# Optimization experiments

Measured on AMD Instinct MI355X. Metric: run time of the kernel, lower is better.

## Reference

```python
import jax, jax.numpy as jnp
import numpy as np

B, S, H = 32, 64, 512
ATT = 128


def _window_index_tables(seq_len):
    # Enumerate all contiguous windows of size 2..S, same set (order-independent
    # for the softmax-weighted sum) as the torch double loop.
    starts, ends = [], []
    for w in range(2, seq_len + 1):
        for s in range(0, seq_len - w + 1):
            starts.append(s)
            ends.append(s + w)
    starts = np.asarray(starts, np.int32)
    ends = np.asarray(ends, np.int32)
    widths = ends - starts
    ks = np.floor(np.log2(widths)).astype(np.int32)  # sparse-table level per window
    e2 = ends - (1 << ks)                            # second gather position
    return starts, e2, ks


def setup_inputs() -> dict:
    key = jax.random.key(0)
    k0, k1, k2, k3, k4 = jax.random.split(key, 5)
    return {
        "lstm_out": jax.random.normal(k0, (B, S, H), dtype=jnp.float32),
        "W1": jax.random.normal(k1, (H, ATT), dtype=jnp.float32) * 0.05,
        "b1": jax.random.normal(k2, (ATT,), dtype=jnp.float32) * 0.05,
        "W2": jax.random.normal(k3, (ATT, 1), dtype=jnp.float32) * 0.05,
        "b2": jax.random.normal(k4, (1,), dtype=jnp.float32) * 0.05,
    }


def reference(lstm_out, W1, b1, W2, b2):
    b, s, h = lstm_out.shape
    # Sparse table: M[k][:, i] = max over lstm_out[:, i : i+2^k] (clipped to s).
    n_levels = int(np.floor(np.log2(s))) + 1
    tables = [lstm_out]
    for k in range(1, n_levels):
        half = 1 << (k - 1)
        prev = tables[-1]
        shifted = jnp.concatenate(
            [prev[:, half:], jnp.full((b, half, h), -jnp.inf, prev.dtype)], axis=1)
        tables.append(jnp.maximum(prev, shifted))
    Mstack = jnp.stack(tables)  # [K, B, S, H]

    starts, e2, ks = _window_index_tables(s)
    # Range max of each window = max of two overlapping power-of-two blocks.
    pooled = jnp.maximum(Mstack[ks, :, starts], Mstack[ks, :, e2])  # [n_win, B, H]
    pooled = jnp.transpose(pooled, (1, 0, 2))  # [B, n_win, H]

    hid = jax.nn.relu(jnp.einsum("bnh,ha->bna", pooled, W1) + b1)
    scores = jnp.einsum("bna,ao->bno", hid, W2) + b2  # [B, n_win, 1]
    attn = jax.nn.softmax(scores, axis=1)
    return jnp.sum(attn * pooled, axis=1)  # [B, H]
```

## Files before the change

kernel.cpp:

```cpp
#include <hip/hip_runtime.h>
#include <stdint.h>


typedef unsigned short u16;
typedef unsigned int u32;

#define B_    32
#define S_    64
#define H_    512
#define ATT_  128
#define NWIN  2016
#define NLEV  7
#define TLEV  6

typedef __bf16 bf16x8 __attribute__((ext_vector_type(8)));
typedef float  f32x4  __attribute__((ext_vector_type(4)));

__device__ __forceinline__ float asf(u32 i) {
  union { u32 i; float f; } v; v.i = i; return v.f;
}
__device__ __forceinline__ u32 asu(float f) {
  union { float f; u32 i; } v; v.f = f; return v.i;
}
__device__ __forceinline__ float bf2f(u16 u) { return asf(((u32)u) << 16); }
__device__ __forceinline__ u16 f2bf(float f) {
  u32 i = asu(f);
  i += 0x7fffu + ((i >> 16) & 1u);
  return (u16)(i >> 16);
}
__device__ __forceinline__ u32 bfmax2(u32 a, u32 b) {
  float a0 = asf(a << 16), a1 = asf(a & 0xffff0000u);
  float b0 = asf(b << 16), b1 = asf(b & 0xffff0000u);
  u32 m0 = asu(fmaxf(a0, b0)), m1 = asu(fmaxf(a1, b1));
  return (m1 & 0xffff0000u) | (m0 >> 16);
}
__device__ __forceinline__ uint4 bfmax8(uint4 a, uint4 b) {
  uint4 m;
  m.x = bfmax2(a.x, b.x); m.y = bfmax2(a.y, b.y);
  m.z = bfmax2(a.z, b.z); m.w = bfmax2(a.w, b.w);
  return m;
}
__device__ __forceinline__ bf16x8 as_bf16x8(uint4 v) {
  union { uint4 u; bf16x8 h; } c; c.u = v; return c.h;
}

__launch_bounds__(256)
__global__ void k01_init(const float* __restrict__ lstm, const float* __restrict__ W1,
                         u16* __restrict__ table, u16* __restrict__ w1tf,
                         u16* __restrict__ widx) {
  int bid = blockIdx.x, tid = threadIdx.x;
  __shared__ u16 bufA[64 * 64], bufB[64 * 64];
  if (bid < 256) {
    int hc = bid & 7, b = bid >> 3;
    const float* src = lstm + (size_t)b * S_ * H_ + hc * 64;
    u16* tb = table + (size_t)b * TLEV * S_ * H_ + hc * 64;
    for (int t = tid; t < 64 * 16; t += 256) {
      int r = t >> 4, c4 = t & 15;
      float4 f = *reinterpret_cast<const float4*>(src + r * H_ + c4 * 4);
      ushort4 u;
      u.x = f2bf(f.x); u.y = f2bf(f.y); u.z = f2bf(f.z); u.w = f2bf(f.w);
      *reinterpret_cast<ushort4*>(&bufA[r * 64 + c4 * 4]) = u;
    }
    u16* pa = bufA; u16* pb = bufB;
    for (int k = 1; k < NLEV; ++k) {
      __syncthreads();
      int half = 1 << (k - 1);
      u16* dst_g = tb + (size_t)(k - 1) * S_ * H_;
      for (int t = tid; t < 64 * 16; t += 256) {
        int r = t >> 4, c4 = t & 15;
        int r2 = r + half; if (r2 > 63) r2 = 63;
        uint2 a  = *reinterpret_cast<const uint2*>(&pa[r  * 64 + c4 * 4]);
        uint2 bq = *reinterpret_cast<const uint2*>(&pa[r2 * 64 + c4 * 4]);
        uint2 m; m.x = bfmax2(a.x, bq.x); m.y = bfmax2(a.y, bq.y);
        *reinterpret_cast<uint2*>(&pb[r * 64 + c4 * 4]) = m;
        *reinterpret_cast<uint2*>(dst_g + r * H_ + c4 * 4) = m;
      }
      u16* tmp = pa; pa = pb; pb = tmp;
    }
  } else {
    int gb = bid - 256;
    if (gb == 0) {
      for (int n = tid; n < NWIN; n += 256) {
        int w = 2, rem = n;
        while (rem >= 65 - w) { rem -= 65 - w; ++w; }
        int s = rem;
        int k = 31 - __clz(w);
        int e2 = s + w - (1 << k);
        widx[n] = (u16)(s | (e2 << 6) | (k << 12));
      }
    }
    for (int q = tid; q < 2048; q += 256) {
      int idx = gb * 2048 + q;
      int e = idx & 7, L = (idx >> 3) & 63, j = (idx >> 9) & 7;
      int k2i = (idx >> 12) & 1, kc = idx >> 13;
      int n  = j * 16 + (L & 15);
      int kq = kc * 64 + k2i * 32 + (L >> 4) * 8 + e;
      w1tf[idx] = f2bf(W1[kq * ATT_ + n]);
    }
  }
}

__launch_bounds__(256)
__attribute__((amdgpu_waves_per_eu(1, 4)))
__global__ void k2_scores(const u16* __restrict__ table, const u16* __restrict__ w1tf,
                          const float* __restrict__ b1, const float* __restrict__ w2,
                          const u16* __restrict__ widx, float* __restrict__ scores) {
  const int b = blockIdx.y, mt = blockIdx.x;
  __shared__ u16 Ts[128 * 64];
  __shared__ u16 Bs[8192];
  __shared__ u16 widx_l[64];
  __shared__ float b1s[128], w2s[128];
  int tid = threadIdx.x;
  if (tid < 64) {
    int n = mt * 64 + tid; if (n > NWIN - 1) n = NWIN - 1;
    widx_l[tid] = widx[n];
  }
  if (tid < 128) { b1s[tid] = b1[tid]; w2s[tid] = w2[tid]; }
  __syncthreads();

  const int lv_lo = widx_l[0] >> 12;
  const u16* tb = table + (size_t)b * TLEV * S_ * H_ + (size_t)(lv_lo - 1) * S_ * H_;

  int t0 = tid, t1 = tid + 256, t2 = tid + 512, t3 = tid + 768;
  int r0 = t0 >> 3, r1 = t1 >> 3, r2 = t2 >> 3, r3 = t3 >> 3;
  int c0 = t0 & 7,  c1 = t1 & 7,  c2 = t2 & 7,  c3 = t3 & 7;
  const u16* ts0 = tb + r0 * H_ + c0 * 8;
  const u16* ts1 = tb + r1 * H_ + c1 * 8;
  const u16* ts2 = tb + r2 * H_ + c2 * 8;
  const u16* ts3 = tb + r3 * H_ + c3 * 8;
  int sd0 = r0 * 64 + ((c0 ^ (r0 & 7)) * 8);
  int sd1 = r1 * 64 + ((c1 ^ (r1 & 7)) * 8);
  int sd2 = r2 * 64 + ((c2 ^ (r2 & 7)) * 8);
  int sd3 = r3 * 64 + ((c3 ^ (r3 & 7)) * 8);
  int bo0 = tid * 8, bo1 = bo0 + 2048, bo2 = bo0 + 4096, bo3 = bo0 + 6144;

  int wid = tid >> 6, lane = tid & 63;
  int lrow = lane & 15, quad = lane >> 4;

  int aoff[2][2];
  {
    int pk = widx_l[wid * 16 + lrow];
    int s = pk & 63, e2 = (pk >> 6) & 63, lv = (pk >> 12) - lv_lo;
    int rs = lv * 64 + s, re = lv * 64 + e2;
#pragma unroll
    for (int k2i = 0; k2i < 2; ++k2i) {
      int c = quad + k2i * 4;
      aoff[k2i][0] = rs * 64 + ((c ^ (rs & 7)) * 8);
      aoff[k2i][1] = re * 64 + ((c ^ (re & 7)) * 8);
    }
  }

  uint4 rT0, rT1, rT2, rT3, rB0, rB1, rB2, rB3;

#define ISSUE(KC) do { \
  int kk_ = (KC) * 64; \
  const u16* wsrc_ = w1tf + (KC) * 8192; \
  rT0 = *reinterpret_cast<const uint4*>(ts0 + kk_); \
  rT1 = *reinterpret_cast<const uint4*>(ts1 + kk_); \
  rT2 = *reinterpret_cast<const uint4*>(ts2 + kk_); \
  rT3 = *reinterpret_cast<const uint4*>(ts3 + kk_); \
  rB0 = *reinterpret_cast<const uint4*>(wsrc_ + bo0); \
  rB1 = *reinterpret_cast<const uint4*>(wsrc_ + bo1); \
  rB2 = *reinterpret_cast<const uint4*>(wsrc_ + bo2); \
  rB3 = *reinterpret_cast<const uint4*>(wsrc_ + bo3); \
} while (0)

#define STAGE() do { \
  *reinterpret_cast<uint4*>(&Ts[sd0]) = rT0; \
  *reinterpret_cast<uint4*>(&Ts[sd1]) = rT1; \
  *reinterpret_cast<uint4*>(&Ts[sd2]) = rT2; \
  *reinterpret_cast<uint4*>(&Ts[sd3]) = rT3; \
  *reinterpret_cast<uint4*>(&Bs[bo0]) = rB0; \
  *reinterpret_cast<uint4*>(&Bs[bo1]) = rB1; \
  *reinterpret_cast<uint4*>(&Bs[bo2]) = rB2; \
  *reinterpret_cast<uint4*>(&Bs[bo3]) = rB3; \
} while (0)

  ISSUE(0);

  f32x4 acc[8];
#pragma unroll
  for (int j = 0; j < 8; ++j) acc[j] = (f32x4){0.f, 0.f, 0.f, 0.f};

  for (int kc = 0; kc < 8; ++kc) {
    __syncthreads();
    STAGE();
    __syncthreads();
    if (kc < 7) ISSUE(kc + 1);
#pragma unroll
    for (int k2i = 0; k2i < 2; ++k2i) {
      uint4 va = *reinterpret_cast<const uint4*>(&Ts[aoff[k2i][0]]);
      uint4 vb = *reinterpret_cast<const uint4*>(&Ts[aoff[k2i][1]]);
      bf16x8 af = as_bf16x8(bfmax8(va, vb));
      const u16* bk = &Bs[k2i * 4096 + lane * 8];
#pragma unroll
      for (int j = 0; j < 8; ++j) {
        bf16x8 bfr = *reinterpret_cast<const bf16x8*>(bk + j * 512);
        acc[j] = __builtin_amdgcn_mfma_f32_16x16x32_bf16(af, bfr, acc[j], 0, 0, 0);
      }
    }
  }

#undef ISSUE
#undef STAGE

#pragma unroll
  for (int r = 0; r < 4; ++r) {
    float p = 0.f;
#pragma unroll
    for (int j = 0; j < 8; ++j) {
      int n = j * 16 + lrow;
      float v = acc[j][r] + b1s[n];
      p += (v > 0.f ? v : 0.f) * w2s[n];
    }
    p += __shfl_xor(p, 1, 16);
    p += __shfl_xor(p, 2, 16);
    p += __shfl_xor(p, 4, 16);
    p += __shfl_xor(p, 8, 16);
    if (lrow == 0) {
      int nw = mt * 64 + wid * 16 + quad * 4 + r;
      if (nw < NWIN) scores[b * NWIN + nw] = p;
    }
  }
}

__launch_bounds__(256)
__global__ void k34_out(const u16* __restrict__ table, const float* __restrict__ scores,
                        const u16* __restrict__ widx, float* __restrict__ out) {
  int hc = blockIdx.x, b = blockIdx.y, tid = threadIdx.x;
  __shared__ u16 Tl[6 * 64 * 16];
  __shared__ float attn_l[NWIN];
  __shared__ u16 widx_l[NWIN];
  __shared__ float red[16][16];
  __shared__ float wredM[4], wredS[4];
  const u16* tb = table + (size_t)b * TLEV * S_ * H_;
  int h0 = hc * 16;
  int lane = tid & 63, wid = tid >> 6;

  for (int t = tid; t < 6 * 64 * 2; t += 256) {
    int row = t >> 1, c = t & 1;
    uint4 v = *reinterpret_cast<const uint4*>(tb + row * H_ + h0 + c * 8);
    *reinterpret_cast<uint4*>(&Tl[row * 16 + c * 8]) = v;
  }
  for (int n = tid; n < NWIN; n += 256) widx_l[n] = widx[n];

  float mx = -1e30f;
  for (int n = tid; n < NWIN; n += 256) {
    float v = scores[b * NWIN + n];
    attn_l[n] = v;
    mx = fmaxf(mx, v);
  }
#pragma unroll
  for (int off = 32; off > 0; off >>= 1) mx = fmaxf(mx, __shfl_xor(mx, off, 64));
  if (lane == 0) wredM[wid] = mx;
  __syncthreads();
  mx = fmaxf(fmaxf(wredM[0], wredM[1]), fmaxf(wredM[2], wredM[3]));
  float sum = 0.f;
  for (int n = tid; n < NWIN; n += 256) {
    float e = __expf(attn_l[n] - mx);
    attn_l[n] = e;
    sum += e;
  }
#pragma unroll
  for (int off = 32; off > 0; off >>= 1) sum += __shfl_xor(sum, off, 64);
  if (lane == 0) wredS[wid] = sum;
  __syncthreads();
  float inv = 1.f / (wredS[0] + wredS[1] + wredS[2] + wredS[3]);

  int h = tid & 15, g = tid >> 4;
  float acc = 0.f;
  for (int n = g * 126; n < g * 126 + 126; ++n) {
    int pk = widx_l[n];
    int s = pk & 63, e2 = (pk >> 6) & 63, lv = pk >> 12;
    float va = bf2f(Tl[((lv - 1) * 64 + s) * 16 + h]);
    float vb = bf2f(Tl[((lv - 1) * 64 + e2) * 16 + h]);
    acc += attn_l[n] * fmaxf(va, vb);
  }
  red[g][h] = acc;
  __syncthreads();
  if (tid < 16) {
    float s2 = 0.f;
#pragma unroll
    for (int g2 = 0; g2 < 16; ++g2) s2 += red[g2][tid];
    out[b * H_ + h0 + tid] = s2 * inv;
  }
}

extern "C" void kernel_launch(void* const* d_in, const int* in_sizes, int n_in,
                              void* d_out, int out_size, void* d_ws, size_t ws_size,
                              hipStream_t stream) {
  const float* lstm = (const float*)d_in[0];
  const float* W1   = (const float*)d_in[1];
  const float* b1   = (const float*)d_in[2];
  const float* W2   = (const float*)d_in[3];
  float* out = (float*)d_out;

  char* ws = (char*)d_ws;
  u16*   widx   = (u16*)(ws + 0);
  u16*   w1tf   = (u16*)(ws + 4096);
  u16*   table  = (u16*)(ws + 135168);
  float* scores = (float*)(ws + 12718080);

  k01_init <<<288, 256, 0, stream>>>(lstm, W1, table, w1tf, widx);
  k2_scores<<<dim3(32, B_), 256, 0, stream>>>(table, w1tf, b1, W2, widx, scores);
  k34_out  <<<dim3(32, B_), 256, 0, stream>>>(table, scores, widx, out);
}
```

Measured before the change: 118.1 us.

## Retile score GEMM to 128 windows per block with 2x4 wave grid

The scoring kernel now processes 128 windows per block with 512 threads, arranged as a 4x2 grid of waves (M by N halves). Each wave computes two 16-row M fragments against four N fragments. The per-wave partial scores are combined through shared memory before the store. This halves the number of times each W1 chunk is reloaded per batch and reuses each B fragment across two A fragments. In exchange it has half as many blocks, larger blocks and a higher register count per thread, plus an extra barrier and reduction at the end.

```diff
diff --git a/kernel.cpp b/kernel.cpp
--- a/kernel.cpp
+++ b/kernel.cpp
@@ -100,7 +100,7 @@
   }
 }
 
-__launch_bounds__(256)
+__launch_bounds__(512)
 __attribute__((amdgpu_waves_per_eu(1, 4)))
 __global__ void k2_scores(const u16* __restrict__ table, const u16* __restrict__ w1tf,
                           const float* __restrict__ b1, const float* __restrict__ w2,
@@ -108,79 +108,72 @@
   const int b = blockIdx.y, mt = blockIdx.x;
   __shared__ u16 Ts[128 * 64];
   __shared__ u16 Bs[8192];
-  __shared__ u16 widx_l[64];
+  __shared__ u16 widx_l[128];
   __shared__ float b1s[128], w2s[128];
+  __shared__ float sc2[2][128];
   int tid = threadIdx.x;
-  if (tid < 64) {
-    int n = mt * 64 + tid; if (n > NWIN - 1) n = NWIN - 1;
+  if (tid < 128) {
+    int n = mt * 128 + tid; if (n > NWIN - 1) n = NWIN - 1;
     widx_l[tid] = widx[n];
-  }
-  if (tid < 128) { b1s[tid] = b1[tid]; w2s[tid] = w2[tid]; }
+    b1s[tid] = b1[tid]; w2s[tid] = w2[tid];
+  }
   __syncthreads();
 
   const int lv_lo = widx_l[0] >> 12;
   const u16* tb = table + (size_t)b * TLEV * S_ * H_ + (size_t)(lv_lo - 1) * S_ * H_;
 
-  int t0 = tid, t1 = tid + 256, t2 = tid + 512, t3 = tid + 768;
-  int r0 = t0 >> 3, r1 = t1 >> 3, r2 = t2 >> 3, r3 = t3 >> 3;
-  int c0 = t0 & 7,  c1 = t1 & 7,  c2 = t2 & 7,  c3 = t3 & 7;
+  int t0 = tid, t1 = tid + 512;
+  int r0 = t0 >> 3, r1 = t1 >> 3;
+  int c0 = t0 & 7,  c1 = t1 & 7;
   const u16* ts0 = tb + r0 * H_ + c0 * 8;
   const u16* ts1 = tb + r1 * H_ + c1 * 8;
-  const u16* ts2 = tb + r2 * H_ + c2 * 8;
-  const u16* ts3 = tb + r3 * H_ + c3 * 8;
   int sd0 = r0 * 64 + ((c0 ^ (r0 & 7)) * 8);
   int sd1 = r1 * 64 + ((c1 ^ (r1 & 7)) * 8);
-  int sd2 = r2 * 64 + ((c2 ^ (r2 & 7)) * 8);
-  int sd3 = r3 * 64 + ((c3 ^ (r3 & 7)) * 8);
-  int bo0 = tid * 8, bo1 = bo0 + 2048, bo2 = bo0 + 4096, bo3 = bo0 + 6144;
+  int bo0 = tid * 8, bo1 = bo0 + 4096;
 
   int wid = tid >> 6, lane = tid & 63;
+  int wm = wid & 3, wn = wid >> 2;
   int lrow = lane & 15, quad = lane >> 4;
 
-  int aoff[2][2];
-  {
-    int pk = widx_l[wid * 16 + lrow];
+  int aoff[2][2][2];
+#pragma unroll
+  for (int mi = 0; mi < 2; ++mi) {
+    int pk = widx_l[wm * 32 + mi * 16 + lrow];
     int s = pk & 63, e2 = (pk >> 6) & 63, lv = (pk >> 12) - lv_lo;
     int rs = lv * 64 + s, re = lv * 64 + e2;
 #pragma unroll
     for (int k2i = 0; k2i < 2; ++k2i) {
       int c = quad + k2i * 4;
-      aoff[k2i][0] = rs * 64 + ((c ^ (rs & 7)) * 8);
-      aoff[k2i][1] = re * 64 + ((c ^ (re & 7)) * 8);
-    }
-  }
-
-  uint4 rT0, rT1, rT2, rT3, rB0, rB1, rB2, rB3;
+      aoff[mi][k2i][0] = rs * 64 + ((c ^ (rs & 7)) * 8);
+      aoff[mi][k2i][1] = re * 64 + ((c ^ (re & 7)) * 8);
+    }
+  }
+
+  uint4 rT0, rT1, rB0, rB1;
 
 #define ISSUE(KC) do { \
   int kk_ = (KC) * 64; \
   const u16* wsrc_ = w1tf + (KC) * 8192; \
   rT0 = *reinterpret_cast<const uint4*>(ts0 + kk_); \
   rT1 = *reinterpret_cast<const uint4*>(ts1 + kk_); \
-  rT2 = *reinterpret_cast<const uint4*>(ts2 + kk_); \
-  rT3 = *reinterpret_cast<const uint4*>(ts3 + kk_); \
   rB0 = *reinterpret_cast<const uint4*>(wsrc_ + bo0); \
   rB1 = *reinterpret_cast<const uint4*>(wsrc_ + bo1); \
-  rB2 = *reinterpret_cast<const uint4*>(wsrc_ + bo2); \
-  rB3 = *reinterpret_cast<const uint4*>(wsrc_ + bo3); \
 } while (0)
 
 #define STAGE() do { \
   *reinterpret_cast<uint4*>(&Ts[sd0]) = rT0; \
   *reinterpret_cast<uint4*>(&Ts[sd1]) = rT1; \
-  *reinterpret_cast<uint4*>(&Ts[sd2]) = rT2; \
-  *reinterpret_cast<uint4*>(&Ts[sd3]) = rT3; \
   *reinterpret_cast<uint4*>(&Bs[bo0]) = rB0; \
   *reinterpret_cast<uint4*>(&Bs[bo1]) = rB1; \
-  *reinterpret_cast<uint4*>(&Bs[bo2]) = rB2; \
-  *reinterpret_cast<uint4*>(&Bs[bo3]) = rB3; \
 } while (0)
 
   ISSUE(0);
 
-  f32x4 acc[8];
-#pragma unroll
-  for (int j = 0; j < 8; ++j) acc[j] = (f32x4){0.f, 0.f, 0.f, 0.f};
+  f32x4 acc[2][4];
+#pragma unroll
+  for (int mi = 0; mi < 2; ++mi)
+#pragma unroll
+    for (int j = 0; j < 4; ++j) acc[mi][j] = (f32x4){0.f, 0.f, 0.f, 0.f};
 
   for (int kc = 0; kc < 8; ++kc) {
     __syncthreads();
@@ -189,14 +182,19 @@
     if (kc < 7) ISSUE(kc + 1);
 #pragma unroll
     for (int k2i = 0; k2i < 2; ++k2i) {
-      uint4 va = *reinterpret_cast<const uint4*>(&Ts[aoff[k2i][0]]);
-      uint4 vb = *reinterpret_cast<const uint4*>(&Ts[aoff[k2i][1]]);
-      bf16x8 af = as_bf16x8(bfmax8(va, vb));
-      const u16* bk = &Bs[k2i * 4096 + lane * 8];
-#pragma unroll
-      for (int j = 0; j < 8; ++j) {
+      bf16x8 af[2];
+#pragma unroll
+      for (int mi = 0; mi < 2; ++mi) {
+        uint4 va = *reinterpret_cast<const uint4*>(&Ts[aoff[mi][k2i][0]]);
+        uint4 vb = *reinterpret_cast<const uint4*>(&Ts[aoff[mi][k2i][1]]);
+        af[mi] = as_bf16x8(bfmax8(va, vb));
+      }
+      const u16* bk = &Bs[(k2i * 8 + wn * 4) * 512 + lane * 8];
+#pragma unroll
+      for (int j = 0; j < 4; ++j) {
         bf16x8 bfr = *reinterpret_cast<const bf16x8*>(bk + j * 512);
-        acc[j] = __builtin_amdgcn_mfma_f32_16x16x32_bf16(af, bfr, acc[j], 0, 0, 0);
+        acc[0][j] = __builtin_amdgcn_mfma_f32_16x16x32_bf16(af[0], bfr, acc[0][j], 0, 0, 0);
+        acc[1][j] = __builtin_amdgcn_mfma_f32_16x16x32_bf16(af[1], bfr, acc[1][j], 0, 0, 0);
       }
     }
   }
@@ -205,22 +203,27 @@
 #undef STAGE
 
 #pragma unroll
-  for (int r = 0; r < 4; ++r) {
-    float p = 0.f;
-#pragma unroll
-    for (int j = 0; j < 8; ++j) {
-      int n = j * 16 + lrow;
-      float v = acc[j][r] + b1s[n];
-      p += (v > 0.f ? v : 0.f) * w2s[n];
-    }
-    p += __shfl_xor(p, 1, 16);
-    p += __shfl_xor(p, 2, 16);
-    p += __shfl_xor(p, 4, 16);
-    p += __shfl_xor(p, 8, 16);
-    if (lrow == 0) {
-      int nw = mt * 64 + wid * 16 + quad * 4 + r;
-      if (nw < NWIN) scores[b * NWIN + nw] = p;
-    }
+  for (int mi = 0; mi < 2; ++mi) {
+#pragma unroll
+    for (int r = 0; r < 4; ++r) {
+      float p = 0.f;
+#pragma unroll
+      for (int j = 0; j < 4; ++j) {
+        int n = wn * 64 + j * 16 + lrow;
+        float v = acc[mi][j][r] + b1s[n];
+        p += (v > 0.f ? v : 0.f) * w2s[n];
+      }
+      p += __shfl_xor(p, 1, 16);
+      p += __shfl_xor(p, 2, 16);
+      p += __shfl_xor(p, 4, 16);
+      p += __shfl_xor(p, 8, 16);
+      if (lrow == 0) sc2[wn][wm * 32 + mi * 16 + quad * 4 + r] = p;
+    }
+  }
+  __syncthreads();
+  if (tid < 128) {
+    int nw = mt * 128 + tid;
+    if (nw < NWIN) scores[b * NWIN + nw] = sc2[0][tid] + sc2[1][tid];
   }
 }
 
@@ -302,6 +305,6 @@
   float* scores = (float*)(ws + 12718080);
 
   k01_init <<<288, 256, 0, stream>>>(lstm, W1, table, w1tf, widx);
-  k2_scores<<<dim3(32, B_), 256, 0, stream>>>(table, w1tf, b1, W2, widx, scores);
+  k2_scores<<<dim3(16, B_), 512, 0, stream>>>(table, w1tf, b1, W2, widx, scores);
   k34_out  <<<dim3(32, B_), 256, 0, stream>>>(table, scores, widx, out);
 }
```

Result: no change. 117.3 us (-0.7%).
